# Kernel optimization log

Hardware: AMD Instinct MI355X
Metric: run time of the kernel (lower is better)

The kernel has to match this reference:

```python
import jax, jax.numpy as jnp
import numpy as np

FP8_MAX = 448.0  # float8_e4m3fn max representable value


def _fp8_quant(v):
    """Snap values to the fp8 e4m3 grid (saturating), return fp32."""
    v = jnp.clip(v, -FP8_MAX, FP8_MAX)
    return v.astype(jnp.float8_e4m3fn).astype(jnp.float32)


def setup_inputs() -> dict:
    key = jax.random.key(0)
    k1, k2, k3 = jax.random.split(key, 3)
    N_TOK, D_IN, D_OUT = 8192, 4096, 4096
    x = jax.random.normal(k1, (N_TOK, D_IN), dtype=jnp.float32)
    # weight is stored already quantized to fp8 in the real module; snap to grid
    w = jax.random.normal(k2, (D_OUT, D_IN), dtype=jnp.float32)
    weight_scale = jnp.array([2.0 / FP8_MAX], dtype=jnp.float32)  # per-tensor
    weight = _fp8_quant(w / weight_scale)  # fp8-grid values, kept in fp32
    bias = jax.random.normal(k3, (D_OUT,), dtype=jnp.float32)
    input_scale = jnp.array([4.0 / FP8_MAX], dtype=jnp.float32)  # per-tensor act scale
    return {"x": x, "weight": weight, "weight_scale": weight_scale,
            "bias": bias, "input_scale": input_scale}


def reference(x, weight, weight_scale, bias, input_scale):
    # quantize_activation_per_tensor_fp8: x/scale -> clamp -> fp8 e4m3
    qinput = _fp8_quant(x / input_scale)  # [N, D_in], fp8-grid values
    acc = jnp.einsum('nk,ok->no', qinput, weight)  # fp32 accumulate
    out = acc * (input_scale * weight_scale) + bias
    return out.astype(x.dtype)
```

## Files before the change

kernel.cpp:

```cpp
#include <hip/hip_runtime.h>
#include <stdint.h>

#define FP8_MAX 448.0f

typedef float floatx4 __attribute__((ext_vector_type(4)));
typedef long  longx2  __attribute__((ext_vector_type(2)));

__device__ __forceinline__ void async_copy16(const void* g, void* s) {
    __builtin_amdgcn_global_load_lds(
        (const __attribute__((address_space(1))) void*)g,
        (__attribute__((address_space(3))) void*)s,
        16, 0, 0);
}

__global__ void __launch_bounds__(256) quant_fp8_kernel(
    const float* __restrict__ x, const float* __restrict__ w,
    const float* __restrict__ scale,
    uint8_t* __restrict__ qx, uint8_t* __restrict__ qw,
    long nx4, long ntot4)
{
    const float invx = 1.0f / scale[0];
    const long stride = (long)gridDim.x * 256;
    for (long g = (long)blockIdx.x * 256 + threadIdx.x; g < ntot4; g += stride) {
        const float4* src; int* dst; float inv; long idx;
        if (g < nx4) { src = (const float4*)x; dst = (int*)qx; inv = invx; idx = g; }
        else         { src = (const float4*)w; dst = (int*)qw; inv = 1.0f; idx = g - nx4; }
        float4 v = src[idx];
        float a = fminf(fmaxf(v.x * inv, -FP8_MAX), FP8_MAX);
        float b = fminf(fmaxf(v.y * inv, -FP8_MAX), FP8_MAX);
        float c = fminf(fmaxf(v.z * inv, -FP8_MAX), FP8_MAX);
        float d = fminf(fmaxf(v.w * inv, -FP8_MAX), FP8_MAX);
        int pk = 0;
        pk = __builtin_amdgcn_cvt_pk_fp8_f32(a, b, pk, false);
        pk = __builtin_amdgcn_cvt_pk_fp8_f32(c, d, pk, true);
        dst[idx] = pk;
    }
}

__global__ void __launch_bounds__(256, 2) gemm_fp8_kernel(
    const uint8_t* __restrict__ A, const uint8_t* __restrict__ B,
    const float* __restrict__ bias,
    const float* __restrict__ in_scale, const float* __restrict__ w_scale,
    float* __restrict__ C, int M, int N, int K)
{
    __shared__ __align__(16) uint8_t As[128 * 64];
    __shared__ __align__(16) uint8_t Bs[128 * 64];

    const int tid  = threadIdx.x;
    const int lane = tid & 63;
    const int wid  = tid >> 6;
    const int wm   = wid >> 1;
    const int wn   = wid & 1;
    const int m0   = blockIdx.y * 128;
    const int n0   = blockIdx.x * 128;

    const int mlane = lane & 15;
    const int quad  = lane >> 4;

    const int S0 = tid, S1 = tid + 256;
    const int rA0 = S0 >> 2, cA0 = ((S0 & 3) ^ (rA0 & 3)) * 16;
    const int rA1 = S1 >> 2, cA1 = ((S1 & 3) ^ (rA1 & 3)) * 16;

    const uint8_t* Ab = A + (size_t)m0 * K;
    const uint8_t* Bb = B + (size_t)n0 * K;

    floatx4 acc[4][4];
#pragma unroll
    for (int i = 0; i < 4; ++i)
#pragma unroll
        for (int j = 0; j < 4; ++j) acc[i][j] = (floatx4){0.f, 0.f, 0.f, 0.f};

    const int swz  = (quad ^ (mlane & 3)) * 16;
    const int aoff = (wm * 64 + mlane) * 64 + swz;
    const int boff = (wn * 64 + mlane) * 64 + swz;

    for (int kt = 0; kt < K; kt += 64) {
        async_copy16(Ab + (size_t)rA0 * K + kt + cA0, As + S0 * 16);
        async_copy16(Ab + (size_t)rA1 * K + kt + cA1, As + S1 * 16);
        async_copy16(Bb + (size_t)rA0 * K + kt + cA0, Bs + S0 * 16);
        async_copy16(Bb + (size_t)rA1 * K + kt + cA1, Bs + S1 * 16);
        __syncthreads();

        longx2 av[4], bv[4];
#pragma unroll
        for (int mi = 0; mi < 4; ++mi)
            av[mi] = *(const longx2*)(As + aoff + mi * 1024);
#pragma unroll
        for (int ni = 0; ni < 4; ++ni)
            bv[ni] = *(const longx2*)(Bs + boff + ni * 1024);

#pragma unroll
        for (int mi = 0; mi < 4; ++mi)
#pragma unroll
            for (int ni = 0; ni < 4; ++ni)
                acc[mi][ni] = __builtin_amdgcn_mfma_f32_16x16x32_fp8_fp8(
                    av[mi].x, bv[ni].x, acc[mi][ni], 0, 0, 0);
#pragma unroll
        for (int mi = 0; mi < 4; ++mi)
#pragma unroll
            for (int ni = 0; ni < 4; ++ni)
                acc[mi][ni] = __builtin_amdgcn_mfma_f32_16x16x32_fp8_fp8(
                    av[mi].y, bv[ni].y, acc[mi][ni], 0, 0, 0);

        __syncthreads();
    }

    const float osc = in_scale[0] * w_scale[0];

#pragma unroll
    for (int mi = 0; mi < 4; ++mi) {
#pragma unroll
        for (int ni = 0; ni < 4; ++ni) {
            const int gn = n0 + wn * 64 + ni * 16 + mlane;
            const float bvv = bias[gn];
#pragma unroll
            for (int r = 0; r < 4; ++r) {
                const int gm = m0 + wm * 64 + mi * 16 + quad * 4 + r;
                C[(size_t)gm * N + gn] = acc[mi][ni][r] * osc + bvv;
            }
        }
    }
}

extern "C" void kernel_launch(void* const* d_in, const int* in_sizes, int n_in,
                              void* d_out, int out_size, void* d_ws, size_t ws_size,
                              hipStream_t stream) {
    const float* x        = (const float*)d_in[0];
    const float* weight   = (const float*)d_in[1];
    const float* w_scale  = (const float*)d_in[2];
    const float* bias     = (const float*)d_in[3];
    const float* in_scale = (const float*)d_in[4];
    float* out = (float*)d_out;

    const int N = in_sizes[3];
    const int K = in_sizes[1] / N;
    const int M = in_sizes[0] / K;

    uint8_t* qx = (uint8_t*)d_ws;
    uint8_t* qw = (uint8_t*)d_ws + (size_t)M * K;

    const long nx4   = (long)M * K / 4;
    const long ntot4 = nx4 + (long)N * K / 4;
    long blks = (ntot4 + 255) / 256; if (blks > 2048) blks = 2048;
    quant_fp8_kernel<<<(int)blks, 256, 0, stream>>>(x, weight, in_scale,
                                                    qx, qw, nx4, ntot4);

    dim3 grid(N / 128, M / 128);
    gemm_fp8_kernel<<<grid, 256, 0, stream>>>(qx, qw, bias, in_scale, w_scale,
                                              out, M, N, K);
}
```

Baseline: 435.3 us.

## Switch GEMM to 32x32x64 scaled FP8 MFMA with unit scales

Replaces the 16x16x32 FP8 MFMA tiling (4x4 tiles per wave, two K-halves) with the gfx950 32x32x64 f8f6f4 scaled MFMA using neutral E8M0 scale bytes (0x7F), so each wave issues four larger MFMAs per K-step. LDS fragment loads are rearranged into two 16-byte reads per operand with a matching swizzle, and the epilogue uses the 32x32 output row mapping. The aim is higher MFMA throughput and fewer instruction issues. It risks layout mismatches and possible LDS bank conflicts from the new read pattern.

```diff
diff --git a/kernel.cpp b/kernel.cpp
--- a/kernel.cpp
+++ b/kernel.cpp
@@ -3,8 +3,9 @@
 
 #define FP8_MAX 448.0f
 
-typedef float floatx4 __attribute__((ext_vector_type(4)));
-typedef long  longx2  __attribute__((ext_vector_type(2)));
+typedef float floatx16 __attribute__((ext_vector_type(16)));
+typedef int   intx4    __attribute__((ext_vector_type(4)));
+typedef int   intx8    __attribute__((ext_vector_type(8)));
 
 __device__ __forceinline__ void async_copy16(const void* g, void* s) {
     __builtin_amdgcn_global_load_lds(
@@ -54,8 +55,8 @@
     const int m0   = blockIdx.y * 128;
     const int n0   = blockIdx.x * 128;
 
-    const int mlane = lane & 15;
-    const int quad  = lane >> 4;
+    const int rl = lane & 31;
+    const int h  = lane >> 5;
 
     const int S0 = tid, S1 = tid + 256;
     const int rA0 = S0 >> 2, cA0 = ((S0 & 3) ^ (rA0 & 3)) * 16;
@@ -64,15 +65,20 @@
     const uint8_t* Ab = A + (size_t)m0 * K;
     const uint8_t* Bb = B + (size_t)n0 * K;
 
-    floatx4 acc[4][4];
+    floatx16 acc[2][2];
 #pragma unroll
-    for (int i = 0; i < 4; ++i)
+    for (int i = 0; i < 2; ++i)
 #pragma unroll
-        for (int j = 0; j < 4; ++j) acc[i][j] = (floatx4){0.f, 0.f, 0.f, 0.f};
+        for (int j = 0; j < 2; ++j)
+#pragma unroll
+            for (int r = 0; r < 16; ++r) acc[i][j][r] = 0.f;
 
-    const int swz  = (quad ^ (mlane & 3)) * 16;
-    const int aoff = (wm * 64 + mlane) * 64 + swz;
-    const int boff = (wn * 64 + mlane) * 64 + swz;
+    const int ca   = ((h * 2)     ^ (rl & 3)) * 16;
+    const int cb   = ((h * 2 + 1) ^ (rl & 3)) * 16;
+    const int aoff = (wm * 64 + rl) * 64;
+    const int boff = (wn * 64 + rl) * 64;
+
+    const int sOne = 0x7F7F7F7F;
 
     for (int kt = 0; kt < K; kt += 64) {
         async_copy16(Ab + (size_t)rA0 * K + kt + cA0, As + S0 * 16);
@@ -81,26 +87,30 @@
         async_copy16(Bb + (size_t)rA1 * K + kt + cA1, Bs + S1 * 16);
         __syncthreads();
 
-        longx2 av[4], bv[4];
+        intx8 av[2], bv[2];
 #pragma unroll
-        for (int mi = 0; mi < 4; ++mi)
-            av[mi] = *(const longx2*)(As + aoff + mi * 1024);
+        for (int mi = 0; mi < 2; ++mi) {
+            intx4 lo = *(const intx4*)(As + aoff + mi * 2048 + ca);
+            intx4 hi = *(const intx4*)(As + aoff + mi * 2048 + cb);
+            av[mi] = (intx8){lo[0], lo[1], lo[2], lo[3],
+                             hi[0], hi[1], hi[2], hi[3]};
+        }
 #pragma unroll
-        for (int ni = 0; ni < 4; ++ni)
-            bv[ni] = *(const longx2*)(Bs + boff + ni * 1024);
+        for (int ni = 0; ni < 2; ++ni) {
+            intx4 lo = *(const intx4*)(Bs + boff + ni * 2048 + ca);
+            intx4 hi = *(const intx4*)(Bs + boff + ni * 2048 + cb);
+            bv[ni] = (intx8){lo[0], lo[1], lo[2], lo[3],
+                             hi[0], hi[1], hi[2], hi[3]};
+        }
 
 #pragma unroll
-        for (int mi = 0; mi < 4; ++mi)
+        for (int mi = 0; mi < 2; ++mi)
 #pragma unroll
-            for (int ni = 0; ni < 4; ++ni)
-                acc[mi][ni] = __builtin_amdgcn_mfma_f32_16x16x32_fp8_fp8(
-                    av[mi].x, bv[ni].x, acc[mi][ni], 0, 0, 0);
-#pragma unroll
-        for (int mi = 0; mi < 4; ++mi)
-#pragma unroll
-            for (int ni = 0; ni < 4; ++ni)
-                acc[mi][ni] = __builtin_amdgcn_mfma_f32_16x16x32_fp8_fp8(
-                    av[mi].y, bv[ni].y, acc[mi][ni], 0, 0, 0);
+            for (int ni = 0; ni < 2; ++ni)
+                acc[mi][ni] = __builtin_amdgcn_mfma_scale_f32_32x32x64_f8f6f4(
+                    av[mi], bv[ni], acc[mi][ni],
+                    0 , 0 ,
+                    0, sOne, 0, sOne);
 
         __syncthreads();
     }
@@ -108,14 +118,15 @@
     const float osc = in_scale[0] * w_scale[0];
 
 #pragma unroll
-    for (int mi = 0; mi < 4; ++mi) {
+    for (int mi = 0; mi < 2; ++mi) {
 #pragma unroll
-        for (int ni = 0; ni < 4; ++ni) {
-            const int gn = n0 + wn * 64 + ni * 16 + mlane;
+        for (int ni = 0; ni < 2; ++ni) {
+            const int gn = n0 + wn * 64 + ni * 32 + rl;
             const float bvv = bias[gn];
 #pragma unroll
-            for (int r = 0; r < 4; ++r) {
-                const int gm = m0 + wm * 64 + mi * 16 + quad * 4 + r;
+            for (int r = 0; r < 16; ++r) {
+                const int row = (r & 3) + 8 * (r >> 2) + 4 * h;
+                const int gm = m0 + wm * 64 + mi * 32 + row;
                 C[(size_t)gm * N + gn] = acc[mi][ni][r] * osc + bvv;
             }
         }
```

New measurement: 420.3 us. 3.5% less time.
